# Kernel optimization log

Hardware: AMD Instinct MI355X
Metric: run time of the kernel (lower is better)

## Reference

```python
import jax, jax.numpy as jnp
import numpy as np

BN_EPS = 1e-3


def _bn(x, gamma, beta):
    # training-mode BatchNorm1d: per-call batch statistics (biased variance)
    m = jnp.mean(x, axis=0)
    v = jnp.mean(jnp.square(x - m), axis=0)
    return gamma * (x - m) * jax.lax.rsqrt(v + BN_EPS) + beta


def setup_inputs() -> dict:
    key = jax.random.key(0)
    ks = jax.random.split(key, 8)
    N, V, Cin, Cout = 1_000_000, 100_000, 16, 64
    return {
        "feat": jax.random.normal(ks[0], (V, Cin), dtype=jnp.float32),
        "points_xyz": jax.random.normal(ks[1], (N, Cin), dtype=jnp.float32),
        "unq_inv": jax.random.randint(ks[2], (N,), 0, V),
        "W_pre": jax.random.normal(ks[3], (Cin, Cout), dtype=jnp.float32) * (1.0 / np.sqrt(Cin)),
        "b_pre": jnp.zeros((Cout,), dtype=jnp.float32),
        "gamma_pre": jnp.ones((Cout,), dtype=jnp.float32),
        "beta_pre": jnp.zeros((Cout,), dtype=jnp.float32),
        "W_pos": jax.random.normal(ks[4], (Cout, Cout), dtype=jnp.float32) * (1.0 / np.sqrt(Cout)),
        "b_pos": jnp.zeros((Cout,), dtype=jnp.float32),
        "gamma_n": jnp.ones((Cout,), dtype=jnp.float32),
        "beta_n": jnp.zeros((Cout,), dtype=jnp.float32),
    }


def reference(feat, points_xyz, unq_inv, W_pre, b_pre, gamma_pre, beta_pre,
              W_pos, b_pos, gamma_n, beta_n):
    V = feat.shape[0]
    # per-point branch: pre_mix (Linear + BN), sin/cos gating, scatter-add to voxels
    p = _bn(points_xyz @ W_pre + b_pre, gamma_pre, beta_pre)      # [N, Cout]
    pw = p @ W_pos + b_pos                                        # [N, Cout]
    feat_add_sin = jax.ops.segment_sum(p * jnp.sin(pw), unq_inv, num_segments=V)  # [V, Cout]
    feat_add_cos = jax.ops.segment_sum(p * jnp.cos(pw), unq_inv, num_segments=V)
    # per-voxel (center) branch through the SAME pre_mix / pos_weight layers
    f = _bn(feat @ W_pre + b_pre, gamma_pre, beta_pre)            # [V, Cout]
    mw = f @ W_pos + b_pos
    center_sin = f * jnp.sin(mw)
    center_cos = f * jnp.cos(mw)
    final = (feat_add_sin + center_sin) * center_sin + (feat_add_cos + center_cos) * center_cos
    return jax.nn.relu(_bn(final, gamma_n, beta_n))
```

## Files before the change

kernel.cpp:

```cpp
#include <hip/hip_runtime.h>
#include <cstdint>
#include <cstddef>

constexpr int CIN  = 16;
constexpr int COUT = 64;
constexpr int NMOM = 16 + 136;
constexpr double BN_EPS = 1e-3;

typedef float v2f __attribute__((ext_vector_type(2)));
typedef __fp16 v2h __attribute__((ext_vector_type(2)));
constexpr float INV_2PI = 0.15915494309189535f;

constexpr int P_A = 0, P_B = 64, P_C = 128, P_WC = 192, P_SZ = 192 + CIN * COUT;

constexpr int CHUNK = 512;
constexpr int MB = 256;

__device__ __forceinline__ unsigned bc_u(v2h h) { return __builtin_bit_cast(unsigned, h); }
__device__ __forceinline__ v2h bc_h(unsigned u) { return __builtin_bit_cast(v2h, u); }

__global__ __launch_bounds__(256, 2) void moments2_kernel(const float* __restrict__ xyz, int n1,
                                                       const float* __restrict__ feat, int n2,
                                                       const int* __restrict__ unq,
                                                       int* __restrict__ cnt,
                                                       int* __restrict__ slot32,
                                                       float* __restrict__ partP,
                                                       float* __restrict__ partF)
{
    const int bb  = blockIdx.x;
    const bool second = (bb >= MB);
    const float* x = second ? feat : xyz;
    const int    n = second ? n2 : n1;
    float* part    = second ? partF : partP;
    const int blk  = second ? bb - MB : bb;

    float acc[NMOM];
#pragma unroll
    for (int i = 0; i < NMOM; i++) acc[i] = 0.f;

    int tid = blk * 256 + threadIdx.x;
    int stride = MB * 256;
    for (int r = tid; r < n; r += stride) {
        const float4* xp = (const float4*)(x + (size_t)r * CIN);
        float4 a0 = xp[0], a1 = xp[1], a2 = xp[2], a3 = xp[3];
        if (!second) slot32[r] = atomicAdd(cnt + unq[r], 1);
        float v[16] = {a0.x,a0.y,a0.z,a0.w, a1.x,a1.y,a1.z,a1.w,
                       a2.x,a2.y,a2.z,a2.w, a3.x,a3.y,a3.z,a3.w};
#pragma unroll
        for (int i = 0; i < 16; i++) acc[i] += v[i];
        int c = 16;
#pragma unroll
        for (int k = 0; k < 16; k++)
#pragma unroll
            for (int l = k; l < 16; l++) { acc[c] = fmaf(v[k], v[l], acc[c]); c++; }
    }

    const int lane = threadIdx.x & 63;
    const int wid  = threadIdx.x >> 6;
    float r0 = 0.f, r1 = 0.f, r2 = 0.f;
#pragma unroll
    for (int i = 0; i < NMOM; i++) {
        float s = acc[i];
#pragma unroll
        for (int off = 1; off < 64; off <<= 1) s += __shfl_xor(s, off, 64);
        if (i < 64)       { if (lane == i)       r0 = s; }
        else if (i < 128) { if (lane == i - 64)  r1 = s; }
        else              { if (lane == i - 128) r2 = s; }
    }

    __shared__ float red[4][NMOM];
    red[wid][lane] = r0;
    red[wid][64 + lane] = r1;
    if (lane < NMOM - 128) red[wid][128 + lane] = r2;
    __syncthreads();
    int t = threadIdx.x;
    if (t < NMOM) {
        float s = red[0][t] + red[1][t] + red[2][t] + red[3][t];
        part[(size_t)blk * NMOM + t] = s;
    }
}

__global__ __launch_bounds__(256) void prep_scanA(const float* __restrict__ Wpre, const float* __restrict__ bpre,
                            const float* __restrict__ gpre, const float* __restrict__ bepre,
                            const float* __restrict__ Wpos, const float* __restrict__ bpos,
                            const float* __restrict__ partP, const float* __restrict__ partF,
                            int nrows, int Np, int Vv,
                            float* __restrict__ prepP, float* __restrict__ prepF,
                            const int* __restrict__ cnt, int V,
                            int* __restrict__ chunkSum)
{
    const int t = threadIdx.x;
    const int lane = t & 63, wid = t >> 6;

    if (blockIdx.x >= 2) {
        const int b = blockIdx.x - 2;
        int base = b * CHUNK;
        int i0 = base + t * 2, i1 = i0 + 1;
        int s = ((i0 < V) ? cnt[i0] : 0) + ((i1 < V) ? cnt[i1] : 0);
        __shared__ int redc[4];
#pragma unroll
        for (int off = 1; off < 64; off <<= 1) s += __shfl_xor(s, off, 64);
        if (lane == 0) redc[wid] = s;
        __syncthreads();
        if (t == 0) chunkSum[b] = redc[0] + redc[1] + redc[2] + redc[3];
        return;
    }

    const int br = blockIdx.x;
    const float* part = br ? partF : partP;
    const double n    = br ? (double)Vv : (double)Np;
    const double inv_n = 1.0 / n;
    float* prep       = br ? prepF : prepP;

    __shared__ float sWpre[CIN * 64];
    __shared__ float sWpos[64 * 64];
    __shared__ double mom[NMOM];
    __shared__ double sS[64], sB[64];

    for (int i = t; i < CIN * 64; i += 256) sWpre[i] = Wpre[i];
    for (int i = t; i < 64 * 64; i += 256)  sWpos[i] = Wpos[i];

    if (t < NMOM) {
        double s0 = 0, s1 = 0, s2 = 0, s3 = 0, s4 = 0, s5 = 0, s6 = 0, s7 = 0;
        int r = 0;
        for (; r + 8 <= nrows; r += 8) {
            s0 += (double)part[(size_t)(r + 0) * NMOM + t];
            s1 += (double)part[(size_t)(r + 1) * NMOM + t];
            s2 += (double)part[(size_t)(r + 2) * NMOM + t];
            s3 += (double)part[(size_t)(r + 3) * NMOM + t];
            s4 += (double)part[(size_t)(r + 4) * NMOM + t];
            s5 += (double)part[(size_t)(r + 5) * NMOM + t];
            s6 += (double)part[(size_t)(r + 6) * NMOM + t];
            s7 += (double)part[(size_t)(r + 7) * NMOM + t];
        }
        for (; r < nrows; r++) s0 += (double)part[(size_t)r * NMOM + t];
        mom[t] = ((s0 + s1) + (s2 + s3)) + ((s4 + s5) + (s6 + s7));
    }
    __syncthreads();

    if (t < 64) {
        const int k = t;
        double mu[16];
#pragma unroll
        for (int i = 0; i < 16; i++) mu[i] = mom[i] * inv_n;
        double w[16];
#pragma unroll
        for (int i = 0; i < 16; i++) w[i] = (double)sWpre[i * 64 + k];

        double mk = (double)bpre[k];
#pragma unroll
        for (int i = 0; i < 16; i++) mk += mu[i] * w[i];

        double var = 0.0;
        int c = 16;
#pragma unroll
        for (int a = 0; a < 16; a++)
#pragma unroll
            for (int l = a; l < 16; l++) {
                double cov = mom[c] * inv_n - mu[a] * mu[l]; c++;
                var += (a == l ? 1.0 : 2.0) * w[a] * w[l] * cov;
            }

        double s_k = (double)gpre[k] / sqrt(var + BN_EPS);
        double B_k = (double)bepre[k] + s_k * ((double)bpre[k] - mk);
        sS[k] = s_k; sB[k] = B_k;
    }
    __syncthreads();

    if (t < 64) {
        const int k = t;
        double c0 = (double)bpos[k], c1 = 0.0;
        for (int j = 0; j < 64; j += 2) {
            c0 += sB[j]     * (double)sWpos[j * 64 + k];
            c1 += sB[j + 1] * (double)sWpos[(j + 1) * 64 + k];
        }
        prep[P_A + k] = (float)sS[k];
        prep[P_B + k] = (float)sB[k];
        prep[P_C + k] = (float)(c0 + c1);
    }

    {
        const int k  = t & 63;
        const int i0 = t >> 6;
        for (int i = i0; i < 16; i += 4) {
            double w0 = 0.0, w1 = 0.0;
            for (int j = 0; j < 64; j += 2) {
                w0 += (double)sWpre[i * 64 + j]     * sS[j]     * (double)sWpos[j * 64 + k];
                w1 += (double)sWpre[i * 64 + j + 1] * sS[j + 1] * (double)sWpos[(j + 1) * 64 + k];
            }
            prep[P_WC + i * 64 + k] = (float)(w0 + w1);
        }
    }
}

__global__ __launch_bounds__(64) void scanC(const int* __restrict__ cnt, int V, int N,
                                            const int* __restrict__ chunkSum,
                                            int* __restrict__ start)
{
    const int b = blockIdx.x;
    const int lane = threadIdx.x;

    int pv = 0;
    for (int i = lane; i < b; i += 64) pv += chunkSum[i];
#pragma unroll
    for (int off = 1; off < 64; off <<= 1) pv += __shfl_xor(pv, off, 64);
    const int chunkBase = pv;

    const int base = b * CHUNK + lane * 8;
    int e[8];
    int run = 0;
#pragma unroll
    for (int j = 0; j < 8; j++) {
        int idx = base + j;
        int c = (idx < V) ? cnt[idx] : 0;
        e[j] = run;
        run += c;
    }
    int incl = run;
#pragma unroll
    for (int off = 1; off < 64; off <<= 1) {
        int vv = __shfl_up(incl, off, 64);
        if (lane >= off) incl += vv;
    }
    int excl = incl - run;
    int myBase = chunkBase + excl;
#pragma unroll
    for (int j = 0; j < 8; j++) {
        int idx = base + j;
        if (idx < V) start[idx] = myBase + e[j];
    }
    if (b == 0 && lane == 0) start[V] = N;
}

__global__ __launch_bounds__(256) void scatter_kernel(const int* __restrict__ unq,
                                                      const int* __restrict__ slot32,
                                                      int N, int V,
                                                      const int* __restrict__ start,
                                                      int* __restrict__ sortedIdx)
{
    const int qsz = (V + 3) >> 2;
    const int t0 = blockIdx.x * blockDim.x + threadIdx.x;
    const int stride = gridDim.x * blockDim.x;
    for (int k = 0; k < 4; k++) {
        const int lo = k * qsz;
        const int hi = min(lo + qsz, V);
        for (int t = t0; t < N; t += stride) {
            int v = unq[t];
            if (v >= lo && v < hi)
                sortedIdx[start[v] + slot32[t]] = t;
        }
    }
}

__global__ __launch_bounds__(256) void fused_pass(const float* __restrict__ xyz,
                                                  const float* __restrict__ feat,
                                                  const int* __restrict__ sortedIdx,
                                                  const int* __restrict__ start,
                                                  const float* __restrict__ Wpre,
                                                  const float* __restrict__ prepP,
                                                  const float* __restrict__ prepF,
                                                  float* __restrict__ outFinal,
                                                  float* __restrict__ statsPart, int V)
{
    const int lane = threadIdx.x & 63;
    const int wid  = threadIdx.x >> 6;
    const int rq   = lane >> 2;
    const int cc   = lane & 3;

    __shared__ uint2 ldsq[4][3][64];
    __shared__ unsigned sWcF2[8 * 64];
    uint2* bufA = ldsq[wid][0];
    uint2* bufB = ldsq[wid][1];
    uint2* remb = ldsq[wid][2];
    const int wslot = rq * 4 + cc;

    for (int i = threadIdx.x; i < 8 * 64; i += 256) {
        int fi = i >> 6, ch = i & 63;
        sWcF2[i] = bc_u(__builtin_amdgcn_cvt_pkrtz(prepF[P_WC + (2 * fi) * 64 + ch],
                                                   prepF[P_WC + (2 * fi + 1) * 64 + ch]));
    }
    __syncthreads();

    v2h wpre2[8], wcp2[8];
#pragma unroll
    for (int i = 0; i < 8; i++) {
        wpre2[i] = __builtin_amdgcn_cvt_pkrtz(Wpre[(2 * i) * 64 + lane],
                                              Wpre[(2 * i + 1) * 64 + lane]);
        wcp2[i]  = __builtin_amdgcn_cvt_pkrtz(prepP[P_WC + (2 * i) * 64 + lane],
                                              prepP[P_WC + (2 * i + 1) * 64 + lane]);
    }

    const float AP = prepP[P_A + lane], BP = prepP[P_B + lane];
    const float CPr = prepP[P_C + lane] * INV_2PI;
    const float AF = prepF[P_A + lane], BF = prepF[P_B + lane];
    const float CFr = prepF[P_C + lane] * INV_2PI;

    const int wave = __builtin_amdgcn_readfirstlane((int)((blockIdx.x * blockDim.x + threadIdx.x) >> 6));
    const int nw   = (gridDim.x * blockDim.x) >> 6;
    float s1 = 0.f, s2 = 0.f;

    auto prefetch = [&](int v, int& sb, int& m, uint2& u) {
        sb = __builtin_amdgcn_readfirstlane(start[v]);
        int se = __builtin_amdgcn_readfirstlane(start[v + 1]);
        m = se - sb;
        int ms0 = min(m, 15);
        int row = min(rq, ms0);
        int ridx = sortedIdx[sb + row];
        const float* bp = (row == ms0) ? (feat + (size_t)v * CIN)
                                       : (xyz  + (size_t)ridx * CIN);
        float4 q = *(const float4*)(bp + cc * 4);
        u.x = bc_u(__builtin_amdgcn_cvt_pkrtz(q.x, q.y));
        u.y = bc_u(__builtin_amdgcn_cvt_pkrtz(q.z, q.w));
    };

    auto pointmath = [&](const uint2* buf, int j, v2f& acc) {
        uint4 a = ((const uint4*)buf)[j * 2 + 0];
        uint4 b = ((const uint4*)buf)[j * 2 + 1];
        v2h xs[8] = {bc_h(a.x), bc_h(a.y), bc_h(a.z), bc_h(a.w),
                     bc_h(b.x), bc_h(b.y), bc_h(b.z), bc_h(b.w)};
        float dx = 0.f, dw = 0.f;
#pragma unroll
        for (int i = 0; i < 8; i++) {
            dx = __builtin_amdgcn_fdot2(xs[i], wpre2[i], dx, false);
            dw = __builtin_amdgcn_fdot2(xs[i], wcp2[i],  dw, false);
        }
        float p  = fmaf(AP, dx, BP);
        float r  = fmaf(dw, INV_2PI, CPr);
        float sv = __builtin_amdgcn_sinf(r);
        float cv = __builtin_amdgcn_cosf(r);
        acc += p * (v2f){sv, cv};
    };

    int v = wave;
    int sb = 0, m = 0;
    uint2* cur = bufA;
    uint2* nxt = bufB;
    if (v < V) {
        uint2 u; prefetch(v, sb, m, u);
        cur[wslot] = u;
    }

    while (v < V) {
        const int vn = v + nw;
        int sbn = 0, mn = 0; uint2 un = {};
        if (vn < V) prefetch(vn, sbn, mn, un);

        const int ms0 = min(m, 15);
        v2f acc = (v2f){0.f, 0.f};

        for (int j = 0; j < ms0; j++) pointmath(cur, j, acc);

        for (int base = 15; base < m; base += 16) {
            const int msr  = min(16, m - base);
            const int rowc = min(rq, msr - 1);
            int ridx = sortedIdx[sb + base + rowc];
            float4 q = *(const float4*)(xyz + (size_t)ridx * CIN + cc * 4);
            uint2 u;
            u.x = bc_u(__builtin_amdgcn_cvt_pkrtz(q.x, q.y));
            u.y = bc_u(__builtin_amdgcn_cvt_pkrtz(q.z, q.w));
            remb[wslot] = u;
            for (int j = 0; j < msr; j++) pointmath(remb, j, acc);
        }

        {
            uint4 a = ((const uint4*)cur)[ms0 * 2 + 0];
            uint4 b = ((const uint4*)cur)[ms0 * 2 + 1];
            v2h xs[8] = {bc_h(a.x), bc_h(a.y), bc_h(a.z), bc_h(a.w),
                         bc_h(b.x), bc_h(b.y), bc_h(b.z), bc_h(b.w)};
            float dx = 0.f, dw = 0.f;
#pragma unroll
            for (int i = 0; i < 8; i++) {
                dx = __builtin_amdgcn_fdot2(xs[i], wpre2[i], dx, false);
                dw = __builtin_amdgcn_fdot2(xs[i], bc_h(sWcF2[i * 64 + lane]), dw, false);
            }
            float f  = fmaf(AF, dx, BF);
            float r  = fmaf(dw, INV_2PI, CFr);
            float sv = __builtin_amdgcn_sinf(r);
            float cv = __builtin_amdgcn_cosf(r);
            float cs = f * sv, ccn = f * cv;
            float fin = fmaf(acc.x + cs, cs, (acc.y + ccn) * ccn);
            outFinal[(size_t)v * 64 + lane] = fin;
            s1 += fin;
            s2 = fmaf(fin, fin, s2);
        }

        if (vn < V) nxt[wslot] = un;
        uint2* tmp = cur; cur = nxt; nxt = tmp;
        v = vn; sb = sbn; m = mn;
    }

    __shared__ float sh1[4][64], sh2[4][64];
    sh1[wid][lane] = s1; sh2[wid][lane] = s2;
    __syncthreads();
    if (threadIdx.x < 64) {
        float t1 = sh1[0][lane] + sh1[1][lane] + sh1[2][lane] + sh1[3][lane];
        float t2 = sh2[0][lane] + sh2[1][lane] + sh2[2][lane] + sh2[3][lane];
        float* row = statsPart + (size_t)(blockIdx.x & 63) * 128;
        atomicAdd(row + lane, t1);
        atomicAdd(row + 64 + lane, t2);
    }
}

__global__ __launch_bounds__(256) void norm_kernel(float* __restrict__ out,
                                                   const float* __restrict__ sp,
                                                   const float* __restrict__ gn,
                                                   const float* __restrict__ bnb,
                                                   int V, size_t n4)
{
    __shared__ float sNs[64], sNb[64];
    const int t = threadIdx.x;
    if (t < 64) {
        double u1 = 0.0, u2 = 0.0;
#pragma unroll 4
        for (int r = 0; r < 64; r++) {
            u1 += (double)sp[(size_t)r * 128 + t];
            u2 += (double)sp[(size_t)r * 128 + 64 + t];
        }
        double mean = u1 / (double)V;
        double var  = u2 / (double)V - mean * mean;
        double ns   = (double)gn[t] / sqrt(var + BN_EPS);
        sNs[t] = (float)ns;
        sNb[t] = (float)((double)bnb[t] - ns * mean);
    }
    __syncthreads();

    const float4* ns4 = (const float4*)sNs;
    const float4* nb4 = (const float4*)sNb;
    float4* o4 = (float4*)out;
    size_t i = (size_t)blockIdx.x * blockDim.x + threadIdx.x;
    size_t stride = (size_t)gridDim.x * blockDim.x;
    for (; i < n4; i += stride) {
        int g = (int)(i & 15);
        float4 sc = ns4[g], bi = nb4[g];
        float4 w = o4[i];
        w.x = fmaxf(0.f, fmaf(sc.x, w.x, bi.x));
        w.y = fmaxf(0.f, fmaf(sc.y, w.y, bi.y));
        w.z = fmaxf(0.f, fmaf(sc.z, w.z, bi.z));
        w.w = fmaxf(0.f, fmaf(sc.w, w.w, bi.w));
        o4[i] = w;
    }
}

extern "C" void kernel_launch(void* const* d_in, const int* in_sizes, int n_in,
                              void* d_out, int out_size, void* d_ws, size_t ws_size,
                              hipStream_t stream)
{
    const float* feat  = (const float*)d_in[0];
    const float* xyz   = (const float*)d_in[1];
    const int*   unq   = (const int*)d_in[2];
    const float* Wpre  = (const float*)d_in[3];
    const float* bpre  = (const float*)d_in[4];
    const float* gpre  = (const float*)d_in[5];
    const float* bepre = (const float*)d_in[6];
    const float* Wpos  = (const float*)d_in[7];
    const float* bpos  = (const float*)d_in[8];
    const float* gn    = (const float*)d_in[9];
    const float* bnb   = (const float*)d_in[10];

    const int V = in_sizes[0] / CIN;
    const int N = in_sizes[1] / CIN;
    const int nch = (V + CHUNK - 1) / CHUNK;

    char* ws = (char*)d_ws;
    size_t off = 0;
    auto alloc = [&](size_t bytes) { void* p = ws + off; off += (bytes + 255) & ~size_t(255); return p; };

    int*   cnt       = (int*)alloc((size_t)V * 4);
    float* statsPart = (float*)alloc(64 * 128 * 4);
    const size_t zeroBytes = off;

    int*   slot32    = (int*)alloc((size_t)N * 4);
    int*   start     = (int*)alloc((size_t)(V + 1) * 4);
    int*   chunkSum  = (int*)alloc(256 * 4);
    int*   sortedIdx = (int*)alloc((size_t)(N + 64) * 4);

    float* partP = (float*)alloc((size_t)MB * NMOM * 4);
    float* partF = (float*)alloc((size_t)MB * NMOM * 4);
    float* prepP = (float*)alloc(P_SZ * 4);
    float* prepF = (float*)alloc(P_SZ * 4);

    hipMemsetAsync(d_ws, 0, zeroBytes, stream);

    moments2_kernel<<<2 * MB, 256, 0, stream>>>(xyz, N, feat, V, unq, cnt, slot32, partP, partF);
    prep_scanA<<<nch + 2, 256, 0, stream>>>(Wpre, bpre, gpre, bepre, Wpos, bpos,
                                            partP, partF, MB, N, V, prepP, prepF,
                                            cnt, V, chunkSum);
    scanC<<<nch, 64, 0, stream>>>(cnt, V, N, chunkSum, start);
    scatter_kernel<<<1024, 256, 0, stream>>>(unq, slot32, N, V, start, sortedIdx);
    fused_pass<<<2048, 256, 0, stream>>>(xyz, feat, sortedIdx, start, Wpre,
                                         prepP, prepF, (float*)d_out, statsPart, V);
    norm_kernel<<<512, 256, 0, stream>>>((float*)d_out, statsPart, gn, bnb, V,
                                         (size_t)out_size / 4);
}
```

Baseline: 187.8 us.

## Interleave two voxels per wave in fused pass for more ILP

Each wavefront now handles two voxels at once. It runs their per-point dot-product and sin/cos accumulations interleaved, and double-buffers prefetches for both. The next-iteration buffers double as scratch for points past the first fifteen. The grid is halved to match, and launch bounds ask for 8 blocks per CU. The aim is to hide LDS, trig and gather latency with independent work, at the cost of more registers and LDS and uneven work when the two voxels differ in point count.

```diff
diff --git a/kernel.cpp b/kernel.cpp
--- a/kernel.cpp
+++ b/kernel.cpp
@@ -252,7 +252,7 @@
     }
 }
 
-__global__ __launch_bounds__(256) void fused_pass(const float* __restrict__ xyz,
+__global__ __launch_bounds__(256, 8) void fused_pass(const float* __restrict__ xyz,
                                                   const float* __restrict__ feat,
                                                   const int* __restrict__ sortedIdx,
                                                   const int* __restrict__ start,
@@ -267,11 +267,8 @@
     const int rq   = lane >> 2;
     const int cc   = lane & 3;
 
-    __shared__ uint2 ldsq[4][3][64];
+    __shared__ uint2 ldsq[4][4][64];
     __shared__ unsigned sWcF2[8 * 64];
-    uint2* bufA = ldsq[wid][0];
-    uint2* bufB = ldsq[wid][1];
-    uint2* remb = ldsq[wid][2];
     const int wslot = rq * 4 + cc;
 
     for (int i = threadIdx.x; i < 8 * 64; i += 256) {
@@ -297,6 +294,7 @@
 
     const int wave = __builtin_amdgcn_readfirstlane((int)((blockIdx.x * blockDim.x + threadIdx.x) >> 6));
     const int nw   = (gridDim.x * blockDim.x) >> 6;
+    const int stride2 = nw * 2;
     float s1 = 0.f, s2 = 0.f;
 
     auto prefetch = [&](int v, int& sb, int& m, uint2& u) {
@@ -331,25 +329,7 @@
         acc += p * (v2f){sv, cv};
     };
 
-    int v = wave;
-    int sb = 0, m = 0;
-    uint2* cur = bufA;
-    uint2* nxt = bufB;
-    if (v < V) {
-        uint2 u; prefetch(v, sb, m, u);
-        cur[wslot] = u;
-    }
-
-    while (v < V) {
-        const int vn = v + nw;
-        int sbn = 0, mn = 0; uint2 un = {};
-        if (vn < V) prefetch(vn, sbn, mn, un);
-
-        const int ms0 = min(m, 15);
-        v2f acc = (v2f){0.f, 0.f};
-
-        for (int j = 0; j < ms0; j++) pointmath(cur, j, acc);
-
+    auto remainder = [&](int sb, int m, v2f& acc, uint2* scratch) {
         for (int base = 15; base < m; base += 16) {
             const int msr  = min(16, m - base);
             const int rowc = min(rq, msr - 1);
@@ -358,35 +338,73 @@
             uint2 u;
             u.x = bc_u(__builtin_amdgcn_cvt_pkrtz(q.x, q.y));
             u.y = bc_u(__builtin_amdgcn_cvt_pkrtz(q.z, q.w));
-            remb[wslot] = u;
-            for (int j = 0; j < msr; j++) pointmath(remb, j, acc);
-        }
-
-        {
-            uint4 a = ((const uint4*)cur)[ms0 * 2 + 0];
-            uint4 b = ((const uint4*)cur)[ms0 * 2 + 1];
-            v2h xs[8] = {bc_h(a.x), bc_h(a.y), bc_h(a.z), bc_h(a.w),
-                         bc_h(b.x), bc_h(b.y), bc_h(b.z), bc_h(b.w)};
-            float dx = 0.f, dw = 0.f;
-#pragma unroll
-            for (int i = 0; i < 8; i++) {
-                dx = __builtin_amdgcn_fdot2(xs[i], wpre2[i], dx, false);
-                dw = __builtin_amdgcn_fdot2(xs[i], bc_h(sWcF2[i * 64 + lane]), dw, false);
-            }
-            float f  = fmaf(AF, dx, BF);
-            float r  = fmaf(dw, INV_2PI, CFr);
-            float sv = __builtin_amdgcn_sinf(r);
-            float cv = __builtin_amdgcn_cosf(r);
-            float cs = f * sv, ccn = f * cv;
-            float fin = fmaf(acc.x + cs, cs, (acc.y + ccn) * ccn);
-            outFinal[(size_t)v * 64 + lane] = fin;
-            s1 += fin;
-            s2 = fmaf(fin, fin, s2);
-        }
-
-        if (vn < V) nxt[wslot] = un;
-        uint2* tmp = cur; cur = nxt; nxt = tmp;
-        v = vn; sb = sbn; m = mn;
+            scratch[wslot] = u;
+            for (int j = 0; j < msr; j++) pointmath(scratch, j, acc);
+        }
+    };
+
+    auto centerout = [&](const uint2* buf, int ms0, const v2f& acc, int v) {
+        uint4 a = ((const uint4*)buf)[ms0 * 2 + 0];
+        uint4 b = ((const uint4*)buf)[ms0 * 2 + 1];
+        v2h xs[8] = {bc_h(a.x), bc_h(a.y), bc_h(a.z), bc_h(a.w),
+                     bc_h(b.x), bc_h(b.y), bc_h(b.z), bc_h(b.w)};
+        float dx = 0.f, dw = 0.f;
+#pragma unroll
+        for (int i = 0; i < 8; i++) {
+            dx = __builtin_amdgcn_fdot2(xs[i], wpre2[i], dx, false);
+            dw = __builtin_amdgcn_fdot2(xs[i], bc_h(sWcF2[i * 64 + lane]), dw, false);
+        }
+        float f  = fmaf(AF, dx, BF);
+        float r  = fmaf(dw, INV_2PI, CFr);
+        float sv = __builtin_amdgcn_sinf(r);
+        float cv = __builtin_amdgcn_cosf(r);
+        float cs = f * sv, ccn = f * cv;
+        float fin = fmaf(acc.x + cs, cs, (acc.y + ccn) * ccn);
+        outFinal[(size_t)v * 64 + lane] = fin;
+        s1 += fin;
+        s2 = fmaf(fin, fin, s2);
+    };
+
+    int v0 = wave * 2, v1 = v0 + 1;
+    int sb0 = 0, m0 = 0, sb1 = 0, m1 = 0;
+    uint2* cur0 = ldsq[wid][0];
+    uint2* cur1 = ldsq[wid][1];
+    uint2* nxt0 = ldsq[wid][2];
+    uint2* nxt1 = ldsq[wid][3];
+    if (v0 < V) { uint2 u; prefetch(v0, sb0, m0, u); cur0[wslot] = u; }
+    if (v1 < V) { uint2 u; prefetch(v1, sb1, m1, u); cur1[wslot] = u; }
+
+    while (v0 < V) {
+        const int v0n = v0 + stride2, v1n = v0n + 1;
+        int sb0n = 0, m0n = 0, sb1n = 0, m1n = 0;
+        uint2 u0n = {}, u1n = {};
+        if (v0n < V) prefetch(v0n, sb0n, m0n, u0n);
+        if (v1n < V) prefetch(v1n, sb1n, m1n, u1n);
+
+        const bool has1 = (v1 < V);
+        const int ms0a = min(m0, 15);
+        const int ms0b = has1 ? min(m1, 15) : 0;
+        const int mc = min(ms0a, ms0b);
+        v2f accA = (v2f){0.f, 0.f}, accB = (v2f){0.f, 0.f};
+
+        for (int j = 0; j < mc; j++) {
+            pointmath(cur0, j, accA);
+            pointmath(cur1, j, accB);
+        }
+        for (int j = mc; j < ms0a; j++) pointmath(cur0, j, accA);
+        for (int j = mc; j < ms0b; j++) pointmath(cur1, j, accB);
+
+        if (m0 > 15)          remainder(sb0, m0, accA, nxt0);
+        if (has1 && m1 > 15)  remainder(sb1, m1, accB, nxt1);
+
+        centerout(cur0, ms0a, accA, v0);
+        if (has1) centerout(cur1, ms0b, accB, v1);
+
+        if (v0n < V) nxt0[wslot] = u0n;
+        if (v1n < V) nxt1[wslot] = u1n;
+        uint2* t0 = cur0; cur0 = nxt0; nxt0 = t0;
+        uint2* t1 = cur1; cur1 = nxt1; nxt1 = t1;
+        v0 = v0n; v1 = v1n; sb0 = sb0n; m0 = m0n; sb1 = sb1n; m1 = m1n;
     }
 
     __shared__ float sh1[4][64], sh2[4][64];
@@ -487,7 +505,7 @@
                                             cnt, V, chunkSum);
     scanC<<<nch, 64, 0, stream>>>(cnt, V, N, chunkSum, start);
     scatter_kernel<<<1024, 256, 0, stream>>>(unq, slot32, N, V, start, sortedIdx);
-    fused_pass<<<2048, 256, 0, stream>>>(xyz, feat, sortedIdx, start, Wpre,
+    fused_pass<<<1024, 256, 0, stream>>>(xyz, feat, sortedIdx, start, Wpre,
                                          prepP, prepF, (float*)d_out, statsPart, V);
     norm_kernel<<<512, 256, 0, stream>>>((float*)d_out, statsPart, gn, bnb, V,
                                          (size_t)out_size / 4);
```

After: 198.2 us. 1.06x slower.
